# Kernel tuning notes

Measured on AMD Instinct MI355X. Metric: run time of the kernel, lower is better.

The kernel has to match this reference:

```python
import jax, jax.numpy as jnp
import numpy as np

H, W = 2048, 2048          # grid shape (init arg `shape`)
N = H * W
MEAN_MODULO = 1.0


def _conv2d_valid(x, k):
    """x: [1,1,H,W], k: [3,3] fixed finite-difference kernel. Valid padding, stride 1."""
    return jax.lax.conv_general_dilated(x, k.reshape(1, 1, 3, 3), (1, 1), 'VALID')


def setup_inputs() -> dict:
    key = jax.random.key(0)
    k1, k2, k3 = jax.random.split(key, 3)
    pred_E = jax.random.uniform(k1, (N,), jnp.float32)          # E > 0 (divisor via sum conv)
    pred_v = jax.random.uniform(k2, (N,), jnp.float32)          # Poisson ratio in [0,1)
    strain = jax.random.normal(k3, (N, 3), jnp.float32)         # [exx, eyy, exy] per point
    return {"pred_E": pred_E, "pred_v": pred_v, "strain": strain}


def reference(pred_E, pred_v, strain):
    # --- calculate_stress ---
    # Original builds C(v) per row from v.detach().numpy(): the matmul part uses a
    # detached v, while the E/(1-v^2) fraction keeps gradient flow through v.
    vd = jax.lax.stop_gradient(pred_v)
    # strain[i] @ [[1,v,0],[v,1,0],[0,0,(1-v)/2]] , vectorized over all rows
    m_xx = strain[:, 0] + vd * strain[:, 1]
    m_yy = vd * strain[:, 0] + strain[:, 1]
    m_xy = strain[:, 2] * (1.0 - vd) * 0.5
    frac = pred_E / (1.0 - jnp.square(pred_v))   # gradient flows through pred_v here
    s_xx = m_xx * frac
    s_yy = m_yy * frac
    s_xy = m_xy * frac

    # --- calculate_loss_r ---
    sum_k = jnp.ones((3, 3), jnp.float32)
    wx_xx = jnp.array([[-1., -1., -1.], [0., 0., 0.], [1., 1., 1.]], jnp.float32)
    wx_xy = jnp.array([[1., 0., -1.], [1., 0., -1.], [1., 0., -1.]], jnp.float32)
    wy_yy = wx_xy   # same stencil values as in source
    wy_xy = wx_xx

    E_conv = _conv2d_valid(pred_E.reshape(1, 1, H, W), sum_k)
    fx = (_conv2d_valid(s_xx.reshape(1, 1, H, W), wx_xx)
          + _conv2d_valid(s_xy.reshape(1, 1, H, W), wx_xy))
    fy = (_conv2d_valid(s_yy.reshape(1, 1, H, W), wy_yy)
          + _conv2d_valid(s_xy.reshape(1, 1, H, W), wy_xy))

    loss_x = jnp.mean(jnp.abs(fx / E_conv))
    loss_y = jnp.mean(jnp.abs(fy / E_conv))
    loss_e = jnp.abs(jnp.mean(pred_E) - MEAN_MODULO)
    return loss_x + loss_y + loss_e / 100.0
```

## Files before the change

kernel.cpp:

```cpp
#include <hip/hip_runtime.h>

#define GH 2048
#define GW 2048
#define OH 2046
#define OW 2046

constexpr int TILE = 32;
constexpr int HALO = 34;
constexpr int GRID_X = 64;
constexpr int GRID_Y = 64;
constexpr int NBLOCKS = GRID_X * GRID_Y;

__global__ __launch_bounds__(256)
void stencil_kernel(const float* __restrict__ E, const float* __restrict__ v,
                    const float* __restrict__ strain, float2* __restrict__ partials) {
    __shared__ float sE [HALO][HALO + 1];
    __shared__ float sxx[HALO][HALO + 1];
    __shared__ float syy[HALO][HALO + 1];
    __shared__ float sxy[HALO][HALO + 1];
    __shared__ float wsum[4][2];

    const int tileX = blockIdx.x * TILE;
    const int tileY = blockIdx.y * TILE;
    const int t = threadIdx.y * 32 + threadIdx.x;

    for (int p = t; p < HALO * HALO; p += 256) {
        int ly = p / HALO, lx = p - ly * HALO;
        int gi = tileY + ly, gj = tileX + lx;
        float e = 0.f, sx = 0.f, sy = 0.f, sz = 0.f;
        if (gi < GH && gj < GW) {
            int idx = gi * GW + gj;
            e = E[idx];
            float vv  = v[idx];
            float exx = strain[idx * 3 + 0];
            float eyy = strain[idx * 3 + 1];
            float exy = strain[idx * 3 + 2];
            float frac = e / (1.f - vv * vv);
            sx = (exx + vv * eyy) * frac;
            sy = (vv * exx + eyy) * frac;
            sz = exy * (1.f - vv) * 0.5f * frac;
        }
        sE [ly][lx] = e;
        sxx[ly][lx] = sx;
        syy[ly][lx] = sy;
        sxy[ly][lx] = sz;
    }
    __syncthreads();

    float acc = 0.f;
    float eacc = 0.f;
    for (int r = threadIdx.y; r < TILE; r += 8) {
        int y = r, x = threadIdx.x;
        eacc += sE[y][x];
        int oi = tileY + r, oj = tileX + threadIdx.x;
        if (oi < OH && oj < OW) {
            float Ec = 0.f;
            #pragma unroll
            for (int di = 0; di < 3; ++di)
                #pragma unroll
                for (int dj = 0; dj < 3; ++dj)
                    Ec += sE[y + di][x + dj];
            float fx = (sxx[y + 2][x] + sxx[y + 2][x + 1] + sxx[y + 2][x + 2])
                     - (sxx[y    ][x] + sxx[y    ][x + 1] + sxx[y    ][x + 2])
                     + (sxy[y][x]     + sxy[y + 1][x]     + sxy[y + 2][x])
                     - (sxy[y][x + 2] + sxy[y + 1][x + 2] + sxy[y + 2][x + 2]);
            float fy = (syy[y][x]     + syy[y + 1][x]     + syy[y + 2][x])
                     - (syy[y][x + 2] + syy[y + 1][x + 2] + syy[y + 2][x + 2])
                     + (sxy[y + 2][x] + sxy[y + 2][x + 1] + sxy[y + 2][x + 2])
                     - (sxy[y    ][x] + sxy[y    ][x + 1] + sxy[y    ][x + 2]);
            float inv = 1.f / Ec;
            acc += fabsf(fx * inv) + fabsf(fy * inv);
        }
    }
    #pragma unroll
    for (int off = 32; off > 0; off >>= 1) {
        acc  += __shfl_down(acc,  off, 64);
        eacc += __shfl_down(eacc, off, 64);
    }
    const int wave = t >> 6;
    if ((t & 63) == 0) { wsum[wave][0] = acc; wsum[wave][1] = eacc; }
    __syncthreads();
    if (t == 0) {
        float a = wsum[0][0] + wsum[1][0] + wsum[2][0] + wsum[3][0];
        float e = wsum[0][1] + wsum[1][1] + wsum[2][1] + wsum[3][1];
        partials[blockIdx.y * GRID_X + blockIdx.x] = make_float2(a, e);
    }
}

__global__ __launch_bounds__(256)
void finalize_kernel(const float2* __restrict__ partials, float* __restrict__ out) {
    __shared__ double sacc[4][2];
    double a = 0.0, e = 0.0;
    for (int i = threadIdx.x; i < NBLOCKS; i += 256) {
        float2 p = partials[i];
        a += (double)p.x;
        e += (double)p.y;
    }
    #pragma unroll
    for (int off = 32; off > 0; off >>= 1) {
        a += __shfl_down(a, off, 64);
        e += __shfl_down(e, off, 64);
    }
    const int wave = threadIdx.x >> 6;
    if ((threadIdx.x & 63) == 0) { sacc[wave][0] = a; sacc[wave][1] = e; }
    __syncthreads();
    if (threadIdx.x == 0) {
        double A = sacc[0][0] + sacc[1][0] + sacc[2][0] + sacc[3][0];
        double Esum = sacc[0][1] + sacc[1][1] + sacc[2][1] + sacc[3][1];
        double M = (double)OH * (double)OW;
        double loss_xy = A / M;
        double loss_e = fabs(Esum / ((double)GH * (double)GW) - 1.0) / 100.0;
        out[0] = (float)(loss_xy + loss_e);
    }
}

extern "C" void kernel_launch(void* const* d_in, const int* in_sizes, int n_in,
                              void* d_out, int out_size, void* d_ws, size_t ws_size,
                              hipStream_t stream) {
    const float* E      = (const float*)d_in[0];
    const float* v      = (const float*)d_in[1];
    const float* strain = (const float*)d_in[2];
    float* out = (float*)d_out;
    float2* partials = (float2*)d_ws;

    hipLaunchKernelGGL(stencil_kernel, dim3(GRID_X, GRID_Y), dim3(32, 8), 0, stream,
                       E, v, strain, partials);
    hipLaunchKernelGGL(finalize_kernel, dim3(1), dim3(256), 0, stream, partials, out);
}
```

Before: 118.8 us.

## Replace shared-memory tiles with per-wave register sliding window and lane shuffles

```diff
diff --git a/kernel.cpp b/kernel.cpp
--- a/kernel.cpp
+++ b/kernel.cpp
@@ -5,93 +5,91 @@
 #define OH 2046
 #define OW 2046
 
-constexpr int TILE = 32;
-constexpr int HALO = 34;
-constexpr int GRID_X = 64;
-constexpr int GRID_Y = 64;
-constexpr int NBLOCKS = GRID_X * GRID_Y;
+constexpr int R      = 33;
+constexpr int BANDS  = 62;
+constexpr int CTILES = 33;
+constexpr int NWAVES = CTILES * BANDS;
+constexpr int NBLOCKS = (NWAVES + 3) / 4;
 
 __global__ __launch_bounds__(256)
 void stencil_kernel(const float* __restrict__ E, const float* __restrict__ v,
                     const float* __restrict__ strain, float2* __restrict__ partials) {
-    __shared__ float sE [HALO][HALO + 1];
-    __shared__ float sxx[HALO][HALO + 1];
-    __shared__ float syy[HALO][HALO + 1];
-    __shared__ float sxy[HALO][HALO + 1];
-    __shared__ float wsum[4][2];
+    const int wid  = blockIdx.x * 4 + (threadIdx.x >> 6);
+    const int lane = threadIdx.x & 63;
+    if (wid >= NWAVES) return;
+    const int tile = wid % CTILES;
+    const int band = wid / CTILES;
+    const int col  = tile * 62 + lane;
+    const int row0 = band * R;
 
-    const int tileX = blockIdx.x * TILE;
-    const int tileY = blockIdx.y * TILE;
-    const int t = threadIdx.y * 32 + threadIdx.x;
+    const bool eown_col = (lane < 62) || (tile == CTILES - 1);
+    const int  own_rows = (band == BANDS - 1) ? R + 2 : R;
+    const bool out_ok   = (lane < 62);
 
-    for (int p = t; p < HALO * HALO; p += 256) {
-        int ly = p / HALO, lx = p - ly * HALO;
-        int gi = tileY + ly, gj = tileX + lx;
-        float e = 0.f, sx = 0.f, sy = 0.f, sz = 0.f;
-        if (gi < GH && gj < GW) {
-            int idx = gi * GW + gj;
-            e = E[idx];
-            float vv  = v[idx];
-            float exx = strain[idx * 3 + 0];
-            float eyy = strain[idx * 3 + 1];
-            float exy = strain[idx * 3 + 2];
-            float frac = e / (1.f - vv * vv);
-            sx = (exx + vv * eyy) * frac;
-            sy = (vv * exx + eyy) * frac;
-            sz = exy * (1.f - vv) * 0.5f * frac;
+    float he0=0, he1=0, he2=0, hxx0=0, hxx1=0, hxx2=0, hxy0=0, hxy1=0, hxy2=0;
+    float sz0=0, sz1=0, sz2=0, sy0=0, sy1=0, sy2=0;
+    float acc = 0.f, eacc = 0.f;
+
+    int idx = row0 * GW + col;
+    float e_n  = E[idx];
+    float v_n  = v[idx];
+    float xx_n = strain[3 * idx + 0];
+    float yy_n = strain[3 * idx + 1];
+    float xy_n = strain[3 * idx + 2];
+
+    for (int k = 0; k < R + 2; ++k) {
+        const float e = e_n, vv = v_n, exx = xx_n, eyy = yy_n, exy = xy_n;
+        if (k < R + 1) {
+            const int idx2 = idx + GW;
+            e_n  = E[idx2];
+            v_n  = v[idx2];
+            xx_n = strain[3 * idx2 + 0];
+            yy_n = strain[3 * idx2 + 1];
+            xy_n = strain[3 * idx2 + 2];
         }
-        sE [ly][lx] = e;
-        sxx[ly][lx] = sx;
-        syy[ly][lx] = sy;
-        sxy[ly][lx] = sz;
+        if (eown_col && k < own_rows) eacc += e;
+
+        const float frac = e / (1.f - vv * vv);
+        const float sx  = (exx + vv * eyy) * frac;
+        const float sy_ = (vv * exx + eyy) * frac;
+        const float sz_ = exy * (1.f - vv) * 0.5f * frac;
+
+        const float he_  = e   + __shfl_down(e,   1, 64) + __shfl_down(e,   2, 64);
+        const float hxx_ = sx  + __shfl_down(sx,  1, 64) + __shfl_down(sx,  2, 64);
+        const float hxy_ = sz_ + __shfl_down(sz_, 1, 64) + __shfl_down(sz_, 2, 64);
+
+        he0 = he1;   he1 = he2;   he2 = he_;
+        hxx0 = hxx1; hxx1 = hxx2; hxx2 = hxx_;
+        hxy0 = hxy1; hxy1 = hxy2; hxy2 = hxy_;
+        sz0 = sz1;   sz1 = sz2;   sz2 = sz_;
+        sy0 = sy1;   sy1 = sy2;   sy2 = sy_;
+
+        if (k >= 2) {
+            const float Vxy = sz0 + sz1 + sz2;
+            const float Vyy = sy0 + sy1 + sy2;
+            const float fx = (hxx2 - hxx0) + Vxy - __shfl_down(Vxy, 2, 64);
+            const float fy = (Vyy - __shfl_down(Vyy, 2, 64)) + (hxy2 - hxy0);
+            const float Ec = he0 + he1 + he2;
+            const float inv = 1.f / Ec;
+            const float c = fabsf(fx * inv) + fabsf(fy * inv);
+            acc += out_ok ? c : 0.f;
+        }
+        idx += GW;
     }
-    __syncthreads();
 
-    float acc = 0.f;
-    float eacc = 0.f;
-    for (int r = threadIdx.y; r < TILE; r += 8) {
-        int y = r, x = threadIdx.x;
-        eacc += sE[y][x];
-        int oi = tileY + r, oj = tileX + threadIdx.x;
-        if (oi < OH && oj < OW) {
-            float Ec = 0.f;
-            #pragma unroll
-            for (int di = 0; di < 3; ++di)
-                #pragma unroll
-                for (int dj = 0; dj < 3; ++dj)
-                    Ec += sE[y + di][x + dj];
-            float fx = (sxx[y + 2][x] + sxx[y + 2][x + 1] + sxx[y + 2][x + 2])
-                     - (sxx[y    ][x] + sxx[y    ][x + 1] + sxx[y    ][x + 2])
-                     + (sxy[y][x]     + sxy[y + 1][x]     + sxy[y + 2][x])
-                     - (sxy[y][x + 2] + sxy[y + 1][x + 2] + sxy[y + 2][x + 2]);
-            float fy = (syy[y][x]     + syy[y + 1][x]     + syy[y + 2][x])
-                     - (syy[y][x + 2] + syy[y + 1][x + 2] + syy[y + 2][x + 2])
-                     + (sxy[y + 2][x] + sxy[y + 2][x + 1] + sxy[y + 2][x + 2])
-                     - (sxy[y    ][x] + sxy[y    ][x + 1] + sxy[y    ][x + 2]);
-            float inv = 1.f / Ec;
-            acc += fabsf(fx * inv) + fabsf(fy * inv);
-        }
-    }
     #pragma unroll
     for (int off = 32; off > 0; off >>= 1) {
         acc  += __shfl_down(acc,  off, 64);
         eacc += __shfl_down(eacc, off, 64);
     }
-    const int wave = t >> 6;
-    if ((t & 63) == 0) { wsum[wave][0] = acc; wsum[wave][1] = eacc; }
-    __syncthreads();
-    if (t == 0) {
-        float a = wsum[0][0] + wsum[1][0] + wsum[2][0] + wsum[3][0];
-        float e = wsum[0][1] + wsum[1][1] + wsum[2][1] + wsum[3][1];
-        partials[blockIdx.y * GRID_X + blockIdx.x] = make_float2(a, e);
-    }
+    if (lane == 0) partials[wid] = make_float2(acc, eacc);
 }
 
 __global__ __launch_bounds__(256)
 void finalize_kernel(const float2* __restrict__ partials, float* __restrict__ out) {
     __shared__ double sacc[4][2];
     double a = 0.0, e = 0.0;
-    for (int i = threadIdx.x; i < NBLOCKS; i += 256) {
+    for (int i = threadIdx.x; i < NWAVES; i += 256) {
         float2 p = partials[i];
         a += (double)p.x;
         e += (double)p.y;
@@ -105,11 +103,11 @@
     if ((threadIdx.x & 63) == 0) { sacc[wave][0] = a; sacc[wave][1] = e; }
     __syncthreads();
     if (threadIdx.x == 0) {
-        double A = sacc[0][0] + sacc[1][0] + sacc[2][0] + sacc[3][0];
+        double A    = sacc[0][0] + sacc[1][0] + sacc[2][0] + sacc[3][0];
         double Esum = sacc[0][1] + sacc[1][1] + sacc[2][1] + sacc[3][1];
         double M = (double)OH * (double)OW;
         double loss_xy = A / M;
-        double loss_e = fabs(Esum / ((double)GH * (double)GW) - 1.0) / 100.0;
+        double loss_e  = fabs(Esum / ((double)GH * (double)GW) - 1.0) / 100.0;
         out[0] = (float)(loss_xy + loss_e);
     }
 }
@@ -123,7 +121,7 @@
     float* out = (float*)d_out;
     float2* partials = (float2*)d_ws;
 
-    hipLaunchKernelGGL(stencil_kernel, dim3(GRID_X, GRID_Y), dim3(32, 8), 0, stream,
+    hipLaunchKernelGGL(stencil_kernel, dim3(NBLOCKS), dim3(256), 0, stream,
                        E, v, strain, partials);
     hipLaunchKernelGGL(finalize_kernel, dim3(1), dim3(256), 0, stream, partials, out);
 }
```

Result: no change. 119.4 us (+0.5%).
